# Kernel tuning notes

Hardware: AMD Instinct MI355X
Metric: run time of the kernel (lower is better)

Reference implementation:

```python
import jax, jax.numpy as jnp
import numpy as np

B, S, D, H = 4, 2048, 1024, 16
HD = D // H
ROPE_THETA = 10000.0


def setup_inputs() -> dict:
    key = jax.random.key(0)
    ks = jax.random.split(key, 5)
    scale = 1.0 / np.sqrt(D)
    inp = {
        "x": jax.random.normal(ks[0], (B, S, D), dtype=jnp.float32),
        "Wq": jax.random.normal(ks[1], (D, D), dtype=jnp.float32) * scale,
        "bq": jnp.zeros((D,), jnp.float32),
        "Wk": jax.random.normal(ks[2], (D, D), dtype=jnp.float32) * scale,
        "bk": jnp.zeros((D,), jnp.float32),
        "Wv": jax.random.normal(ks[3], (D, D), dtype=jnp.float32) * scale,
        "bv": jnp.zeros((D,), jnp.float32),
        "Wo": jax.random.normal(ks[4], (D, D), dtype=jnp.float32) * scale,
        "bo": jnp.zeros((D,), jnp.float32),
        # causal mask: True means masked (j > i), matching masked_fill semantics
        "attn_mask": jnp.triu(jnp.ones((S, S), dtype=bool), k=1),
    }
    return inp


def _rope(x):
    # x: [B, H, S, HD]; half-split rotary embedding
    half = HD // 2
    inv_freq = 1.0 / (ROPE_THETA ** (jnp.arange(0, half, dtype=jnp.float32) / half))
    pos = jnp.arange(x.shape[2], dtype=jnp.float32)
    freqs = pos[:, None] * inv_freq[None, :]            # [S, half]
    cos = jnp.cos(freqs)[None, None]                    # [1,1,S,half]
    sin = jnp.sin(freqs)[None, None]
    x1, x2 = x[..., :half], x[..., half:]
    return jnp.concatenate([x1 * cos - x2 * sin, x2 * cos + x1 * sin], axis=-1)


def reference(x, Wq, bq, Wk, bk, Wv, bv, Wo, bo, attn_mask):
    def shape(t):  # [B,S,D] -> [B,H,S,HD]
        return t.reshape(B, S, H, HD).transpose(0, 2, 1, 3)

    q = shape(x @ Wq.T + bq)
    k = shape(x @ Wk.T + bk)
    v = shape(x @ Wv.T + bv)
    q = _rope(q)
    k = _rope(k)
    scores = jnp.einsum("bhqd,bhkd->bhqk", q, k) * (HD ** -0.5)
    scores = jnp.where(attn_mask[None, None], -jnp.inf, scores)
    w = jax.nn.softmax(scores, axis=-1)
    attn = jnp.einsum("bhqk,bhkd->bhqd", w, v)
    merged = attn.transpose(0, 2, 1, 3).reshape(B, S, D)
    return merged @ Wo.T + bo
```

## Files before the change

### kernel.cpp

```cpp
#include <hip/hip_runtime.h>
#include <math.h>

#define BATCH 4
#define SEQ   2048
#define DMODEL 1024
#define NHEAD 16
#define HDIM  64
#define MROWS (BATCH*SEQ)

typedef unsigned short u16;
typedef unsigned int   u32;

using bf16x8 = __attribute__((ext_vector_type(8))) short;
using f32x4  = __attribute__((ext_vector_type(4))) float;
using f32x16 = __attribute__((ext_vector_type(16))) float;
using u32x4  = __attribute__((ext_vector_type(4))) unsigned int;

__device__ __forceinline__ u16 f2bf(float f) {
    u32 u = __float_as_uint(f);
    u += 0x7fffu + ((u >> 16) & 1u);
    return (u16)(u >> 16);
}
__device__ __forceinline__ u32 pack2bf(float a, float b) {
    u32 ua = __float_as_uint(a); ua += 0x7fffu + ((ua >> 16) & 1u);
    u32 ub = __float_as_uint(b); ub += 0x7fffu + ((ub >> 16) & 1u);
    return (ua >> 16) | (ub & 0xffff0000u);
}
__device__ __forceinline__ u32 cvtpk(float a, float b) {
    u32 r;
    asm("v_cvt_pk_bf16_f32 %0, %1, %2" : "=v"(r) : "v"(a), "v"(b));
    return r;
}
#define PLSWAP(a, b) asm("v_permlane32_swap_b32 %0, %1" : "+v"(a), "+v"(b))

#define GLOBAL_LOAD_LDS16(gp, lp)                                              \
    __builtin_amdgcn_global_load_lds(                                          \
        (const __attribute__((address_space(1))) void*)(gp),                   \
        (__attribute__((address_space(3))) void*)(lp), 16, 0, 0)

__global__ __launch_bounds__(256) void convert_inputs(
    const float* __restrict__ x,  const float* __restrict__ wq,
    const float* __restrict__ wk, const float* __restrict__ wv,
    const float* __restrict__ wo, u16* __restrict__ dst)
{
    long long i4 = ((long long)blockIdx.x * 256 + threadIdx.x) * 4;
    const float* src; long long off;
    if (i4 < 8388608LL) { src = x; off = i4; }
    else {
        long long j = i4 - 8388608LL;
        int seg = (int)(j >> 20);
        off = j & 1048575LL;
        src = (seg == 0) ? wq : (seg == 1) ? wk : (seg == 2) ? wv : wo;
    }
    float4 v = *(const float4*)(src + off);
    u32 lo = (u32)f2bf(v.x) | ((u32)f2bf(v.y) << 16);
    u32 hi = (u32)f2bf(v.z) | ((u32)f2bf(v.w) << 16);
    *(uint2*)(dst + i4) = make_uint2(lo, hi);
}

template<int EPI>
__global__ __launch_bounds__(512) void gemm8(
    const u16* __restrict__ A, const u16* __restrict__ W,
    const float* __restrict__ b0_, const float* __restrict__ b1_,
    u16* __restrict__ C0_, u16* __restrict__ C1_, float* __restrict__ Cf)
{
    __shared__ __align__(16) u16 smem[65536];

    const int t    = threadIdx.x;
    const int lane = t & 63;
    const int w    = t >> 6;
    const int quad = lane >> 4;
    const int l15  = lane & 15;
    const int wm   = w >> 2;
    const int wn   = w & 3;

    const int bx  = blockIdx.x;
    const int xcd = bx & 7;
    const int i_  = bx >> 3;
    const int bml = i_ & 3;
    const int n_  = i_ >> 2;

    const int bm = (xcd * 4 + bml) * 256;
    const int bn = n_ * 256;

    const bool   isq  = (EPI == 0) ? (bn < 1024) : true;
    const float* bias = (EPI == 0) ? (isq ? b0_ : b1_) : b0_;
    u16*         Cb   = (EPI == 0) ? (isq ? C0_ : C1_) : C0_;
    const int    bnl  = (EPI == 0) ? (bn & 1023) : bn;

    const int sr8 = lane >> 3;
    const int scl = (lane & 7) ^ sr8;
    const u16* gA = A + (size_t)(bm + 8 * w + sr8) * DMODEL + scl * 8;
    const u16* gB = W + (size_t)(bn + 8 * w + sr8) * DMODEL + scl * 8;

#define STG_A(rg, kt, bs)                                                      \
    GLOBAL_LOAD_LDS16(gA + (size_t)(rg) * 64 * DMODEL + (kt) * 64,             \
                      &smem[(bs) * 16384 + ((rg) * 64 + 8 * w) * 64])
#define STG_B(rg, kt, bs)                                                      \
    GLOBAL_LOAD_LDS16(gB + (size_t)(rg) * 64 * DMODEL + (kt) * 64,             \
                      &smem[32768 + (bs) * 16384 + ((rg) * 64 + 8 * w) * 64])

    STG_B(0, 0, 0); STG_B(1, 0, 0); STG_B(2, 0, 0); STG_B(3, 0, 0);
    STG_A(0, 0, 0); STG_A(2, 0, 0); STG_A(1, 0, 0); STG_A(3, 0, 0);
    STG_B(0, 1, 1); STG_B(1, 1, 1); STG_B(2, 1, 1); STG_B(3, 1, 1);
    STG_A(0, 1, 1); STG_A(2, 1, 1);
    asm volatile("s_waitcnt vmcnt(6)" ::: "memory");
    __builtin_amdgcn_s_barrier();

    const int cA0 = (quad ^ (l15 & 7)) * 8;

    f32x4 acc[8][4] = {};
    bf16x8 bfr[4][2];

#define LOAD_B(Bb) {                                                           \
    _Pragma("unroll")                                                          \
    for (int j = 0; j < 4; ++j) {                                              \
        bfr[j][0] = *(const bf16x8*)&(Bb)[(wn * 64 + 16 * j + l15) * 64 + cA0];\
        bfr[j][1] = *(const bf16x8*)&(Bb)[(wn * 64 + 16 * j + l15) * 64 + (cA0 ^ 32)];\
    } }
#define PHASE(q, Ab, Bb, STAGES, CKPT) {                                       \
    bf16x8 af_[2][2];                                                          \
    if ((q) == 0) LOAD_B(Bb);                                                  \
    _Pragma("unroll")                                                          \
    for (int ii = 0; ii < 2; ++ii) {                                           \
        const int r_ = (wm * 128 + (q) * 32 + 16 * ii + l15) * 64;             \
        af_[ii][0] = *(const bf16x8*)&(Ab)[r_ + cA0];                          \
        af_[ii][1] = *(const bf16x8*)&(Ab)[r_ + (cA0 ^ 32)];                   \
    }                                                                          \
    STAGES;                                                                    \
    __builtin_amdgcn_s_barrier();                                              \
    asm volatile("s_waitcnt lgkmcnt(0)" ::: "memory");                         \
    __builtin_amdgcn_sched_barrier(0);                                         \
    __builtin_amdgcn_s_setprio(1);                                             \
    _Pragma("unroll")                                                          \
    for (int ii = 0; ii < 2; ++ii)                                             \
        _Pragma("unroll")                                                      \
        for (int j = 0; j < 4; ++j) {                                          \
            acc[2*(q)+ii][j] = __builtin_amdgcn_mfma_f32_16x16x32_bf16(        \
                af_[ii][0], bfr[j][0], acc[2*(q)+ii][j], 0, 0, 0);             \
            acc[2*(q)+ii][j] = __builtin_amdgcn_mfma_f32_16x16x32_bf16(        \
                af_[ii][1], bfr[j][1], acc[2*(q)+ii][j], 0, 0, 0);             \
        }                                                                      \
    __builtin_amdgcn_s_setprio(0);                                             \
    CKPT;                                                                      \
    __builtin_amdgcn_s_barrier();                                              \
}

    #pragma unroll 1
    for (int i = 0; i < 8; ++i) {
        const bool st = (i < 7);
        const int  kn = 2 * i + 2, kn3 = 2 * i + 3, ko = 2 * i + 1;
        {
            const u16* Ab = smem;
            const u16* Bb = smem + 32768;
            PHASE(0, Ab, Bb, { STG_A(1, ko, 1); STG_A(3, ko, 1); }, {});
            PHASE(1, Ab, Bb, { if (st) { STG_B(0, kn, 0); STG_B(1, kn, 0); } }, {});
            PHASE(2, Ab, Bb, { if (st) { STG_B(2, kn, 0); STG_B(3, kn, 0); } }, {});
            PHASE(3, Ab, Bb, { if (st) { STG_A(0, kn, 0); STG_A(2, kn, 0); } },
                  { if (st) asm volatile("s_waitcnt vmcnt(6)" ::: "memory");
                    else    asm volatile("s_waitcnt vmcnt(0)" ::: "memory"); });
        }
        {
            const u16* Ab = smem + 16384;
            const u16* Bb = smem + 32768 + 16384;
            PHASE(0, Ab, Bb, { if (st) { STG_A(1, kn, 0); STG_A(3, kn, 0); } }, {});
            PHASE(1, Ab, Bb, { if (st) { STG_B(0, kn3, 1); STG_B(1, kn3, 1); } }, {});
            PHASE(2, Ab, Bb, { if (st) { STG_B(2, kn3, 1); STG_B(3, kn3, 1); } }, {});
            PHASE(3, Ab, Bb, { if (st) { STG_A(0, kn3, 1); STG_A(2, kn3, 1); } },
                  { if (st) asm volatile("s_waitcnt vmcnt(6)" ::: "memory");
                    else    asm volatile("s_waitcnt vmcnt(0)" ::: "memory"); });
        }
    }
#undef PHASE
#undef LOAD_B
#undef STG_A
#undef STG_B

    const int wrow = wm * 128;
    const int wcol = wn * 64;
    float bvv[4];
    #pragma unroll
    for (int j = 0; j < 4; j++) bvv[j] = bias[bnl + wcol + 16 * j + l15];

    if constexpr (EPI == 2) {
        #pragma unroll
        for (int ri = 0; ri < 8; ri++)
            #pragma unroll
            for (int r = 0; r < 4; r++) {
                int mg = bm + wrow + 16 * ri + quad * 4 + r;
                #pragma unroll
                for (int j = 0; j < 4; j++)
                    Cf[(size_t)mg * DMODEL + bn + wcol + 16 * j + l15] = acc[ri][j][r] + bvv[j];
            }
    } else if constexpr (EPI == 1) {
        u16* T = smem;
        #pragma unroll
        for (int ri = 0; ri < 8; ri++) {
            #pragma unroll
            for (int j = 0; j < 4; j++) {
                int col = wrow + 16 * ri + quad * 4;
                int row = wcol + 16 * j + l15;
                u32 lo = pack2bf(acc[ri][j][0] + bvv[j], acc[ri][j][1] + bvv[j]);
                u32 hi = pack2bf(acc[ri][j][2] + bvv[j], acc[ri][j][3] + bvv[j]);
                *(uint2*)((char*)T + row * 512 + ((col * 2) ^ ((row & 7) << 4)))
                    = make_uint2(lo, hi);
            }
        }
        __syncthreads();
        {
            int row = t >> 1, half = t & 1;
            int hgl = (bn + row) >> 6;
            int dl  = (bn + row) & 63;
            int bb  = bm >> 11;
            size_t obase = (((size_t)(bb * NHEAD + hgl)) * HDIM + dl) * SEQ
                         + (bm & (SEQ - 1)) + half * 128;
            #pragma unroll
            for (int k = 0; k < 16; k++) {
                uint4 vv = *(const uint4*)((const char*)T + row * 512
                             + ((half * 256 + k * 16) ^ ((row & 7) << 4)));
                *(uint4*)(Cb + obase + k * 8) = vv;
            }
        }
    } else {
        const float qscale = isq ? 0.18033688011112042f : 1.0f;
        float inv[2];
        #pragma unroll
        for (int j = 0; j < 2; j++) {
            int d = 16 * j + l15;
            inv[j] = exp2f(-(float)d * 0.4152410118609203f);
        }
        #pragma unroll
        for (int ri = 0; ri < 8; ri++)
            #pragma unroll
            for (int r = 0; r < 4; r++) {
                int mg = bm + wrow + 16 * ri + quad * 4 + r;
                int s  = mg & (SEQ - 1);
                #pragma unroll
                for (int j = 0; j < 2; j++) {
                    float f = (float)s * inv[j];
                    float sn, cs;
                    __sincosf(f, &sn, &cs);
                    float a1 = acc[ri][j][r]     + bvv[j];
                    float a2 = acc[ri][j + 2][r] + bvv[j + 2];
                    float o1 = (a1 * cs - a2 * sn) * qscale;
                    float o2 = (a2 * cs + a1 * sn) * qscale;
                    Cb[(size_t)mg * DMODEL + bnl + wcol + 16 * j       + l15] = f2bf(o1);
                    Cb[(size_t)mg * DMODEL + bnl + wcol + 16 * (j + 2) + l15] = f2bf(o2);
                }
            }
    }
}

__global__ __launch_bounds__(256) void attn_mfma(
    const u16* __restrict__ Q, const u16* __restrict__ K,
    const u16* __restrict__ VT, u16* __restrict__ O)
{
    __shared__ __align__(16) u16 smem[16640];
    u16* const Qs  = smem;
    u16* const Ks0 = smem + 8192;
    u16* const Ks1 = smem;
    u16* const Vt0 = smem + 12288;
    u16* const Vt1 = smem + 4096;
    float* const lS = (float*)(smem + 16384);

    const int t    = threadIdx.x;
    const int lane = t & 63;
    const int w    = t >> 6;
    const int l31  = lane & 31;
    const int hl   = lane >> 5;
    const int bid  = blockIdx.x;
    const int bh   = bid & 63;
    const int x_   = bid >> 6, g_ = x_ >> 2, r_ = x_ & 3;
    const int qt   = (g_ == 0) ? 15 - r_ : (g_ == 1) ? 8 + r_
                   : (g_ == 2) ? 4 + r_ : 3 - r_;
    const int h    = bh & (NHEAD - 1);
    const int b    = bh >> 4;
    const int q0   = qt * 128;

    const size_t gbase = ((size_t)b * SEQ) * DMODEL + h * HDIM;
    const size_t vbase = ((size_t)(b * NHEAD + h)) * HDIM * SEQ;

    const int rl  = lane >> 3;
    const int csw = (lane & 7) ^ rl;

    #pragma unroll
    for (int i = 0; i < 4; i++) {
        int row = 32 * w + 8 * i + rl;
        GLOBAL_LOAD_LDS16(Q + gbase + (size_t)(q0 + row) * DMODEL + csw * 8,
                          &Qs[(32 * w + 8 * i) * 64]);
    }
    #pragma unroll
    for (int i = 0; i < 2; i++) {
        int row = 16 * w + 8 * i + rl;
        GLOBAL_LOAD_LDS16(K + gbase + (size_t)row * DMODEL + csw * 8,
                          &Ks0[(16 * w + 8 * i) * 64]);
        GLOBAL_LOAD_LDS16(VT + vbase + (size_t)row * SEQ + csw * 8,
                          &Vt0[(16 * w + 8 * i) * 64]);
    }
    __syncthreads();

    bf16x8 qf[4];
    {
        int row = 32 * w + l31;
        #pragma unroll
        for (int s = 0; s < 4; s++) {
            int c = (hl + 2 * s) ^ (row & 7);
            qf[s] = *(const bf16x8*)&Qs[row * 64 + c * 8];
        }
    }
    __syncthreads();

    float lsum = 0.0f;
    f32x16 oacc[2] = {};
    const int qg   = q0 + 32 * w + l31;
    const int qmax = q0 + 32 * w + 31;

#define QUADRANT(KRH, F0, F1) do {                                             \
    f32x16 s_ = {};                                                            \
    __builtin_amdgcn_s_setprio(1);                                             \
    _Pragma("unroll")                                                          \
    for (int stp_ = 0; stp_ < 4; ++stp_) {                                     \
        int c_ = ((hl + 2 * stp_) ^ (l31 & 7)) * 8;                            \
        bf16x8 ka_ = *(const bf16x8*)&Ksb[(32 * (KRH) + l31) * 64 + c_];       \
        s_ = __builtin_amdgcn_mfma_f32_32x32x16_bf16(ka_, qf[stp_], s_, 0, 0, 0);\
    }                                                                          \
    __builtin_amdgcn_s_setprio(0);                                             \
    if (k0 + 32 * (KRH) + 31 > q0 + 32 * w) {                                  \
        _Pragma("unroll")                                                      \
        for (int rr_ = 0; rr_ < 16; ++rr_) {                                   \
            int krg_ = k0 + 32 * (KRH) + (rr_ & 3) + 8 * (rr_ >> 2) + 4 * hl;  \
            if (krg_ > qg) s_[rr_] = -1e30f;                                   \
        }                                                                      \
    }                                                                          \
    float pv_[16];                                                             \
    _Pragma("unroll")                                                          \
    for (int rr_ = 0; rr_ < 16; ++rr_) pv_[rr_] = __builtin_amdgcn_exp2f(s_[rr_]);\
    lsum += ((pv_[0]+pv_[1])+(pv_[2]+pv_[3])) + ((pv_[4]+pv_[5])+(pv_[6]+pv_[7]))\
          + ((pv_[8]+pv_[9])+(pv_[10]+pv_[11])) + ((pv_[12]+pv_[13])+(pv_[14]+pv_[15]));\
    u32 k01_ = cvtpk(pv_[0], pv_[1]),   k23_ = cvtpk(pv_[2], pv_[3]);          \
    u32 k45_ = cvtpk(pv_[4], pv_[5]),   k67_ = cvtpk(pv_[6], pv_[7]);          \
    u32 k89_ = cvtpk(pv_[8], pv_[9]),   kab_ = cvtpk(pv_[10], pv_[11]);        \
    u32 kcd_ = cvtpk(pv_[12], pv_[13]), kef_ = cvtpk(pv_[14], pv_[15]);        \
    PLSWAP(k01_, k45_); PLSWAP(k23_, k67_);                                    \
    PLSWAP(k89_, kcd_); PLSWAP(kab_, kef_);                                    \
    { union { u32x4 u; bf16x8 v; } c0_; c0_.u = (u32x4){k01_, k23_, k45_, k67_};\
      F0 = c0_.v; }                                                            \
    { union { u32x4 u; bf16x8 v; } c1_; c1_.u = (u32x4){k89_, kab_, kcd_, kef_};\
      F1 = c1_.v; }                                                            \
} while (0)

#define PVSTEP(STP, PF) do {                                                   \
    int c_ = ((hl + 2 * (STP)) ^ (l31 & 7)) * 8;                               \
    bf16x8 v0_ = *(const bf16x8*)&Vtb[l31 * 64 + c_];                          \
    bf16x8 v1_ = *(const bf16x8*)&Vtb[(32 + l31) * 64 + c_];                   \
    oacc[0] = __builtin_amdgcn_mfma_f32_32x32x16_bf16(PF, v0_, oacc[0], 0, 0, 0);\
    oacc[1] = __builtin_amdgcn_mfma_f32_32x32x16_bf16(PF, v1_, oacc[1], 0, 0, 0);\
} while (0)

    const int ktn = 2 * qt + 2;
    for (int kt = 0; kt < ktn; kt++) {
        const int k0 = kt * 64;
        u16* const Ksb = (kt & 1) ? Ks1 : Ks0;
        u16* const Vtb = (kt & 1) ? Vt1 : Vt0;

        if (kt + 1 < ktn) {
            u16* const Ksn = (kt & 1) ? Ks0 : Ks1;
            u16* const Vtn = (kt & 1) ? Vt0 : Vt1;
            const size_t kk0 = (size_t)(kt + 1) * 64;
            #pragma unroll
            for (int i = 0; i < 2; i++) {
                int row = 16 * w + 8 * i + rl;
                GLOBAL_LOAD_LDS16(K + gbase + (kk0 + row) * DMODEL + csw * 8,
                                  &Ksn[(16 * w + 8 * i) * 64]);
                GLOBAL_LOAD_LDS16(VT + vbase + (size_t)row * SEQ + kk0 + csw * 8,
                                  &Vtn[(16 * w + 8 * i) * 64]);
            }
        }

        if (k0 <= qmax) {
            const bool q2 = (k0 + 32 <= qmax);
            bf16x8 pa0, pa1, pa2, pa3;
            QUADRANT(0, pa0, pa1);
            __builtin_amdgcn_s_setprio(1);
            PVSTEP(0, pa0); PVSTEP(1, pa1);
            __builtin_amdgcn_s_setprio(0);
            if (q2) {
                QUADRANT(1, pa2, pa3);
                __builtin_amdgcn_s_setprio(1);
                PVSTEP(2, pa2); PVSTEP(3, pa3);
                __builtin_amdgcn_s_setprio(0);
            }
        }
        asm volatile("s_waitcnt vmcnt(0)" ::: "memory");
        __builtin_amdgcn_s_barrier();
    }
#undef QUADRANT
#undef PVSTEP

    lsum += __shfl_xor(lsum, 32, 64);
    if (lane < 32) lS[32 * w + lane] = lsum;
    __syncthreads();

    #pragma unroll
    for (int g = 0; g < 4; g++) {
        f32x4 lv = *(const f32x4*)&lS[32 * w + 8 * g + 4 * hl];
        #pragma unroll
        for (int rr = 0; rr < 4; rr++) {
            int qg2 = q0 + 32 * w + rr + 8 * g + 4 * hl;
            float inv = 1.0f / lv[rr];
            #pragma unroll
            for (int dh = 0; dh < 2; dh++) {
                float o = oacc[dh][4 * g + rr] * inv;
                O[gbase + (size_t)qg2 * DMODEL + 32 * dh + l31] = f2bf(o);
            }
        }
    }
}

extern "C" void kernel_launch(void* const* d_in, const int* in_sizes, int n_in,
                              void* d_out, int out_size, void* d_ws, size_t ws_size,
                              hipStream_t stream)
{
    const float* x  = (const float*)d_in[0];
    const float* Wq = (const float*)d_in[1];
    const float* bq = (const float*)d_in[2];
    const float* Wk = (const float*)d_in[3];
    const float* bk = (const float*)d_in[4];
    const float* Wv = (const float*)d_in[5];
    const float* bv = (const float*)d_in[6];
    const float* Wo = (const float*)d_in[7];
    const float* bo = (const float*)d_in[8];

    u16* wsp = (u16*)d_ws;
    u16* xb  = wsp;
    u16* Wqb = wsp + 8388608;
    u16* Wkb = Wqb + 1048576;
    u16* Wvb = Wkb + 1048576;
    u16* Wob = Wvb + 1048576;
    u16* Qb  = Wob + 1048576;
    u16* Kb  = Qb + 8388608;
    u16* Vb  = Kb + 8388608;
    u16* Ab  = Vb + 8388608;

    convert_inputs<<<12288, 256, 0, stream>>>(x, Wq, Wk, Wv, Wo, xb);

    gemm8<0><<<256, 512, 0, stream>>>(xb, Wqb, bq, bk, Qb, Kb, nullptr);

    gemm8<1><<<128, 512, 0, stream>>>(xb, Wvb, bv, nullptr, Vb, nullptr, nullptr);

    attn_mfma<<<1024, 256, 0, stream>>>(Qb, Kb, Vb, Ab);

    gemm8<2><<<128, 512, 0, stream>>>(Ab, Wob, bo, nullptr, nullptr, nullptr,
                                      (float*)d_out);
}
```

Baseline: 271.1 us.

## Add 256x128-tile GEMM kernel for V and output projections

Adds a new GEMM kernel with 256x128 output tiles, triple-buffered LDS staging and a simpler two-phase k-loop, used for the V projection and the output projection. These launches now use 256 blocks instead of 128, so the 256 CUs can all be occupied rather than half sitting idle. gemm8 is reduced to the QK RoPE epilogue only. The cost is more redundant A-tile loads, because each A tile is fetched by twice as many blocks.

Result: faster. 256.1 us (-5.5%).

```diff
diff --git a/kernel.cpp b/kernel.cpp
--- a/kernel.cpp
+++ b/kernel.cpp
@@ -83,10 +83,10 @@
     const int bm = (xcd * 4 + bml) * 256;
     const int bn = n_ * 256;
 
-    const bool   isq  = (EPI == 0) ? (bn < 1024) : true;
-    const float* bias = (EPI == 0) ? (isq ? b0_ : b1_) : b0_;
-    u16*         Cb   = (EPI == 0) ? (isq ? C0_ : C1_) : C0_;
-    const int    bnl  = (EPI == 0) ? (bn & 1023) : bn;
+    const bool   isq  = (bn < 1024);
+    const float* bias = isq ? b0_ : b1_;
+    u16*         Cb   = isq ? C0_ : C1_;
+    const int    bnl  = bn & 1023;
 
     const int sr8 = lane >> 3;
     const int scl = (lane & 7) ^ sr8;
@@ -182,72 +182,178 @@
     #pragma unroll
     for (int j = 0; j < 4; j++) bvv[j] = bias[bnl + wcol + 16 * j + l15];
 
-    if constexpr (EPI == 2) {
-        #pragma unroll
-        for (int ri = 0; ri < 8; ri++)
+    const float qscale = isq ? 0.18033688011112042f : 1.0f;
+    float inv[2];
+    #pragma unroll
+    for (int j = 0; j < 2; j++) {
+        int d = 16 * j + l15;
+        inv[j] = exp2f(-(float)d * 0.4152410118609203f);
+    }
+    #pragma unroll
+    for (int ri = 0; ri < 8; ri++)
+        #pragma unroll
+        for (int r = 0; r < 4; r++) {
+            int mg = bm + wrow + 16 * ri + quad * 4 + r;
+            int s  = mg & (SEQ - 1);
+            #pragma unroll
+            for (int j = 0; j < 2; j++) {
+                float f = (float)s * inv[j];
+                float sn, cs;
+                __sincosf(f, &sn, &cs);
+                float a1 = acc[ri][j][r]     + bvv[j];
+                float a2 = acc[ri][j + 2][r] + bvv[j + 2];
+                float o1 = (a1 * cs - a2 * sn) * qscale;
+                float o2 = (a2 * cs + a1 * sn) * qscale;
+                Cb[(size_t)mg * DMODEL + bnl + wcol + 16 * j       + l15] = f2bf(o1);
+                Cb[(size_t)mg * DMODEL + bnl + wcol + 16 * (j + 2) + l15] = f2bf(o2);
+            }
+        }
+}
+
+template<int MODE>
+__global__ __launch_bounds__(512) void gemm_bn128(
+    const u16* __restrict__ A, const u16* __restrict__ W,
+    const float* __restrict__ bias_, u16* __restrict__ Cb, float* __restrict__ Cf)
+{
+    __shared__ u16 As[3 * 256 * 64];
+    __shared__ u16 Ws[3 * 128 * 64];
+
+    const int t    = threadIdx.x;
+    const int lane = t & 63;
+    const int w    = t >> 6;
+    const int quad = lane >> 4;
+    const int l15  = lane & 15;
+
+    const int bx  = blockIdx.x;
+    const int xcd = bx & 7;
+    const int i_  = bx >> 3;
+    const int bml = i_ & 3;
+    const int n_  = i_ >> 2;
+
+    const int bm   = (xcd * 4 + bml) * 256;
+    const int bn   = n_ * 128;
+    const int wrow = (w >> 1) * 64;
+    const int wcol = (w & 1) * 64;
+
+    const int sr8 = lane >> 3;
+    const int scl = (lane & 7) ^ sr8;
+    const u16* gA = A + (size_t)(bm + 8 * w + sr8) * DMODEL + scl * 8;
+    const u16* gB = W + (size_t)(bn + 8 * w + sr8) * DMODEL + scl * 8;
+
+#define STAGE_A(li, kt, bs)                                                    \
+    GLOBAL_LOAD_LDS16(gA + (size_t)(li) * 64 * DMODEL + (kt) * 64,             \
+                      &As[(bs) * 16384 + ((li) * 64 + 8 * w) * 64])
+#define STAGE_B(li, kt, bs)                                                    \
+    GLOBAL_LOAD_LDS16(gB + (size_t)(li) * 64 * DMODEL + (kt) * 64,             \
+                      &Ws[(bs) * 8192 + ((li) * 64 + 8 * w) * 64])
+
+    STAGE_A(0, 0, 0); STAGE_A(1, 0, 0); STAGE_A(2, 0, 0); STAGE_A(3, 0, 0);
+    STAGE_B(0, 0, 0); STAGE_B(1, 0, 0);
+    STAGE_A(0, 1, 1); STAGE_A(1, 1, 1); STAGE_A(2, 1, 1); STAGE_A(3, 1, 1);
+    STAGE_B(0, 1, 1); STAGE_B(1, 1, 1);
+    asm volatile("s_waitcnt vmcnt(6)" ::: "memory");
+    __builtin_amdgcn_s_barrier();
+
+    const int c0 = (quad ^ (l15 & 7)) * 8;
+    const int c1 = c0 ^ 32;
+
+    f32x4 acc[4][4] = {};
+
+    int bsel = 0;
+    #pragma unroll 1
+    for (int kt = 0; kt < DMODEL / 64; ++kt) {
+        const u16* Ab = &As[bsel * 16384];
+        const u16* Bb = &Ws[bsel * 8192];
+        const int  ks = kt + 2;
+        const int  sb = (bsel >= 1) ? bsel - 1 : 2;
+        const bool st = (ks < DMODEL / 64);
+
+        bf16x8 af[4], bfr[4];
+
+        #pragma unroll
+        for (int i = 0; i < 4; ++i)
+            af[i] = *(const bf16x8*)&Ab[(wrow + 16 * i + l15) * 64 + c0];
+        #pragma unroll
+        for (int j = 0; j < 4; ++j)
+            bfr[j] = *(const bf16x8*)&Bb[(wcol + 16 * j + l15) * 64 + c0];
+        if (st) { STAGE_A(0, ks, sb); STAGE_A(1, ks, sb); STAGE_A(2, ks, sb); }
+        __builtin_amdgcn_s_barrier();
+        __builtin_amdgcn_s_setprio(1);
+        #pragma unroll
+        for (int i = 0; i < 4; ++i)
+            #pragma unroll
+            for (int j = 0; j < 4; ++j)
+                acc[i][j] = __builtin_amdgcn_mfma_f32_16x16x32_bf16(af[i], bfr[j], acc[i][j], 0, 0, 0);
+        __builtin_amdgcn_s_setprio(0);
+        __builtin_amdgcn_s_barrier();
+
+        #pragma unroll
+        for (int i = 0; i < 4; ++i)
+            af[i] = *(const bf16x8*)&Ab[(wrow + 16 * i + l15) * 64 + c1];
+        #pragma unroll
+        for (int j = 0; j < 4; ++j)
+            bfr[j] = *(const bf16x8*)&Bb[(wcol + 16 * j + l15) * 64 + c1];
+        if (st) { STAGE_A(3, ks, sb); STAGE_B(0, ks, sb); STAGE_B(1, ks, sb); }
+        __builtin_amdgcn_s_barrier();
+        __builtin_amdgcn_s_setprio(1);
+        #pragma unroll
+        for (int i = 0; i < 4; ++i)
+            #pragma unroll
+            for (int j = 0; j < 4; ++j)
+                acc[i][j] = __builtin_amdgcn_mfma_f32_16x16x32_bf16(af[i], bfr[j], acc[i][j], 0, 0, 0);
+        __builtin_amdgcn_s_setprio(0);
+        if (st) asm volatile("s_waitcnt vmcnt(6)" ::: "memory");
+        else    asm volatile("s_waitcnt vmcnt(0)" ::: "memory");
+        __builtin_amdgcn_s_barrier();
+
+        bsel = (bsel == 2) ? 0 : bsel + 1;
+    }
+#undef STAGE_A
+#undef STAGE_B
+
+    float bv[4];
+    #pragma unroll
+    for (int j = 0; j < 4; j++) bv[j] = bias_[bn + wcol + 16 * j + l15];
+
+    if constexpr (MODE == 0) {
+        #pragma unroll
+        for (int i = 0; i < 4; i++)
             #pragma unroll
             for (int r = 0; r < 4; r++) {
-                int mg = bm + wrow + 16 * ri + quad * 4 + r;
+                int mg = bm + wrow + 16 * i + quad * 4 + r;
                 #pragma unroll
                 for (int j = 0; j < 4; j++)
-                    Cf[(size_t)mg * DMODEL + bn + wcol + 16 * j + l15] = acc[ri][j][r] + bvv[j];
-            }
-    } else if constexpr (EPI == 1) {
-        u16* T = smem;
-        #pragma unroll
-        for (int ri = 0; ri < 8; ri++) {
+                    Cf[(size_t)mg * DMODEL + bn + wcol + 16 * j + l15] = acc[i][j][r] + bv[j];
+            }
+    } else {
+        u16* T = As;
+        #pragma unroll
+        for (int i = 0; i < 4; i++) {
             #pragma unroll
             for (int j = 0; j < 4; j++) {
-                int col = wrow + 16 * ri + quad * 4;
+                int col = wrow + 16 * i + quad * 4;
                 int row = wcol + 16 * j + l15;
-                u32 lo = pack2bf(acc[ri][j][0] + bvv[j], acc[ri][j][1] + bvv[j]);
-                u32 hi = pack2bf(acc[ri][j][2] + bvv[j], acc[ri][j][3] + bvv[j]);
-                *(uint2*)((char*)T + row * 512 + ((col * 2) ^ ((row & 7) << 4)))
+                u32 lo = pack2bf(acc[i][j][0] + bv[j], acc[i][j][1] + bv[j]);
+                u32 hi = pack2bf(acc[i][j][2] + bv[j], acc[i][j][3] + bv[j]);
+                *(uint2*)((char*)T + row * 512 + ((col * 2) ^ ((row & 3) << 4)))
                     = make_uint2(lo, hi);
             }
         }
         __syncthreads();
         {
-            int row = t >> 1, half = t & 1;
-            int hgl = (bn + row) >> 6;
-            int dl  = (bn + row) & 63;
-            int bb  = bm >> 11;
+            int row  = t >> 2, colc = t & 3;
+            int hgl  = (bn + row) >> 6;
+            int dl   = (bn + row) & 63;
+            int bb   = bm >> 11;
             size_t obase = (((size_t)(bb * NHEAD + hgl)) * HDIM + dl) * SEQ
-                         + (bm & (SEQ - 1)) + half * 128;
-            #pragma unroll
-            for (int k = 0; k < 16; k++) {
+                         + (bm & (SEQ - 1)) + colc * 64;
+            #pragma unroll
+            for (int k = 0; k < 8; k++) {
                 uint4 vv = *(const uint4*)((const char*)T + row * 512
-                             + ((half * 256 + k * 16) ^ ((row & 7) << 4)));
+                             + ((colc * 128 + k * 16) ^ ((row & 3) << 4)));
                 *(uint4*)(Cb + obase + k * 8) = vv;
             }
         }
-    } else {
-        const float qscale = isq ? 0.18033688011112042f : 1.0f;
-        float inv[2];
-        #pragma unroll
-        for (int j = 0; j < 2; j++) {
-            int d = 16 * j + l15;
-            inv[j] = exp2f(-(float)d * 0.4152410118609203f);
-        }
-        #pragma unroll
-        for (int ri = 0; ri < 8; ri++)
-            #pragma unroll
-            for (int r = 0; r < 4; r++) {
-                int mg = bm + wrow + 16 * ri + quad * 4 + r;
-                int s  = mg & (SEQ - 1);
-                #pragma unroll
-                for (int j = 0; j < 2; j++) {
-                    float f = (float)s * inv[j];
-                    float sn, cs;
-                    __sincosf(f, &sn, &cs);
-                    float a1 = acc[ri][j][r]     + bvv[j];
-                    float a2 = acc[ri][j + 2][r] + bvv[j + 2];
-                    float o1 = (a1 * cs - a2 * sn) * qscale;
-                    float o2 = (a2 * cs + a1 * sn) * qscale;
-                    Cb[(size_t)mg * DMODEL + bnl + wcol + 16 * j       + l15] = f2bf(o1);
-                    Cb[(size_t)mg * DMODEL + bnl + wcol + 16 * (j + 2) + l15] = f2bf(o2);
-                }
-            }
     }
 }
 
@@ -446,10 +552,9 @@
 
     gemm8<0><<<256, 512, 0, stream>>>(xb, Wqb, bq, bk, Qb, Kb, nullptr);
 
-    gemm8<1><<<128, 512, 0, stream>>>(xb, Wvb, bv, nullptr, Vb, nullptr, nullptr);
+    gemm_bn128<1><<<256, 512, 0, stream>>>(xb, Wvb, bv, Vb, nullptr);
 
     attn_mfma<<<1024, 256, 0, stream>>>(Qb, Kb, Vb, Ab);
 
-    gemm8<2><<<128, 512, 0, stream>>>(Ab, Wob, bo, nullptr, nullptr, nullptr,
-                                      (float*)d_out);
-}
+    gemm_bn128<0><<<256, 512, 0, stream>>>(Ab, Wob, bo, nullptr, (float*)d_out);
+}
```
